# Performance work log

Hardware: AMD Instinct MI355X
Metric: run time of the kernel (lower is better)

## Reference

```python
import jax, jax.numpy as jnp
import numpy as np

T, B, D, N = 2048, 16, 1024, 128
EPS = 1e-6


def setup_inputs() -> dict:
    key = jax.random.key(0)
    ks = jax.random.split(key, 6)
    sc = 1.0 / np.sqrt(D)  # ~xavier scale for [N, D] projections
    x = jax.random.normal(ks[0], (T, B, D), jnp.float32)
    S = jnp.zeros((B, N, N), jnp.float32)
    W_k = jax.random.normal(ks[1], (N, D), jnp.float32) * sc
    W_v = jax.random.normal(ks[2], (N, D), jnp.float32) * sc
    W_q = jax.random.normal(ks[3], (N, D), jnp.float32) * sc
    W_beta = jax.random.normal(ks[4], (N, D), jnp.float32) * sc
    d_beta = jnp.full((N,), 0.1, jnp.float32)
    b_beta = jnp.zeros((N,), jnp.float32)
    return {"x": x, "S": S, "W_k": W_k, "W_v": W_v, "W_q": W_q,
            "W_beta": W_beta, "d_beta": d_beta, "b_beta": b_beta}


def reference(x, S, W_k, W_v, W_q, W_beta, d_beta, b_beta):
    # Batched input projections (dense GEMMs over all T*B tokens at once).
    k_all = jnp.einsum('tbd,nd->tbn', x, W_k)
    v_all = jnp.einsum('tbd,nd->tbn', x, W_v)
    q_all = jnp.einsum('tbd,nd->tbn', x, W_q)
    bx_all = jnp.einsum('tbd,nd->tbn', x, W_beta)

    def step(S, inp):
        k, v, q, bx = inp  # each [B, N]
        k_norm = k / (jnp.linalg.norm(k, axis=-1, keepdims=True) + EPS)
        retrieved = jnp.einsum('bij,bj->bi', S, k_norm)
        beta = jax.nn.sigmoid(bx + d_beta * retrieved + b_beta)
        # Delta rule: S += beta * outer(v - retrieved, k_norm)
        S = S + beta[..., None] * ((v - retrieved)[..., None] * k_norm[:, None, :])
        out = jnp.einsum('bij,bj->bi', S, q)
        out = out * jax.nn.silu(out)  # self-gated output
        return S, out

    S_final, outputs = jax.lax.scan(step, S, (k_all, v_all, q_all, bx_all))
    return outputs, S_final
```

## Files before the change

kernel.cpp:

```cpp
#include <hip/hip_runtime.h>
#include <hip/hip_bf16.h>


#define T_STEPS 2048
#define NB 16
#define ND 128
#define KD 1024
#define PSTRIDE 512

typedef __attribute__((ext_vector_type(4))) float f32x4;
typedef __attribute__((ext_vector_type(2))) float f32x2;
typedef __attribute__((ext_vector_type(8))) short short8v;

__device__ __forceinline__ unsigned short f2bf(float f) {
  union { float f; unsigned int u; } c; c.f = f;
  unsigned int u = c.u;
  unsigned int r = u + 0x7fffu + ((u >> 16) & 1u);
  return (unsigned short)(r >> 16);
}

__global__ __launch_bounds__(256) void proj_gemm(
    const float* __restrict__ X,
    const float* __restrict__ Wk, const float* __restrict__ Wv,
    const float* __restrict__ Wq, const float* __restrict__ Wb,
    float* __restrict__ C)
{
  __shared__ unsigned short As[128 * 64];
  __shared__ unsigned short Bs[128 * 64];
  const int tid = threadIdx.x;
  const int bm = blockIdx.x;
  const int bn = blockIdx.y;
  const float* W = (bn == 0) ? Wk : ((bn == 1) ? Wv : ((bn == 2) ? Wq : Wb));
  const int lane = tid & 63;
  const int wave = tid >> 6;
  const int wr = wave >> 1, wc = wave & 1;

  f32x4 acc[4][4];
#pragma unroll
  for (int i = 0; i < 4; i++)
#pragma unroll
    for (int j = 0; j < 4; j++) acc[i][j] = (f32x4){0.f, 0.f, 0.f, 0.f};

  for (int k0 = 0; k0 < KD; k0 += 64) {
    __syncthreads();
#pragma unroll
    for (int c = 0; c < 4; c++) {
      const int g = tid + c * 256;
      const int row = g >> 3;
      const int ch = g & 7;
      const int pos = ((ch ^ (row & 7)) * 8);
      {
        const float* ga = X + (size_t)(bm * 128 + row) * KD + k0 + ch * 8;
        float4 f0 = *(const float4*)(ga);
        float4 f1 = *(const float4*)(ga + 4);
        union { unsigned short u[8]; short8v v; } pk2;
        pk2.u[0] = f2bf(f0.x); pk2.u[1] = f2bf(f0.y);
        pk2.u[2] = f2bf(f0.z); pk2.u[3] = f2bf(f0.w);
        pk2.u[4] = f2bf(f1.x); pk2.u[5] = f2bf(f1.y);
        pk2.u[6] = f2bf(f1.z); pk2.u[7] = f2bf(f1.w);
        *reinterpret_cast<short8v*>(&As[row * 64 + pos]) = pk2.v;
      }
      {
        const float* gb = W + (size_t)row * KD + k0 + ch * 8;
        float4 f0 = *(const float4*)(gb);
        float4 f1 = *(const float4*)(gb + 4);
        union { unsigned short u[8]; short8v v; } pk2;
        pk2.u[0] = f2bf(f0.x); pk2.u[1] = f2bf(f0.y);
        pk2.u[2] = f2bf(f0.z); pk2.u[3] = f2bf(f0.w);
        pk2.u[4] = f2bf(f1.x); pk2.u[5] = f2bf(f1.y);
        pk2.u[6] = f2bf(f1.z); pk2.u[7] = f2bf(f1.w);
        *reinterpret_cast<short8v*>(&Bs[row * 64 + pos]) = pk2.v;
      }
    }
    __syncthreads();
#pragma unroll
    for (int kk = 0; kk < 2; kk++) {
      const int ch = kk * 4 + (lane >> 4);
      short8v a[4], b[4];
#pragma unroll
      for (int i = 0; i < 4; i++) {
        const int ar = wr * 64 + i * 16 + (lane & 15);
        a[i] = *reinterpret_cast<const short8v*>(&As[ar * 64 + ((ch ^ (ar & 7)) * 8)]);
        const int br = wc * 64 + i * 16 + (lane & 15);
        b[i] = *reinterpret_cast<const short8v*>(&Bs[br * 64 + ((ch ^ (br & 7)) * 8)]);
      }
#pragma unroll
      for (int i = 0; i < 4; i++)
#pragma unroll
        for (int j = 0; j < 4; j++)
          acc[i][j] = __builtin_amdgcn_mfma_f32_16x16x32_bf16(a[i], b[j], acc[i][j], 0, 0, 0);
    }
  }
#pragma unroll
  for (int i = 0; i < 4; i++)
#pragma unroll
    for (int j = 0; j < 4; j++)
#pragma unroll
      for (int r = 0; r < 4; r++) {
        const int row = bm * 128 + wr * 64 + i * 16 + (lane >> 4) * 4 + r;
        const int col = bn * 128 + wc * 64 + j * 16 + (lane & 15);
        C[(size_t)row * PSTRIDE + col] = acc[i][j][r];
      }
}

__global__ __launch_bounds__(256) void norm_k(float* __restrict__ proj) {
  const int lane = threadIdx.x & 63;
  const int wid = (blockIdx.x * 256 + threadIdx.x) >> 6;
  float* rowp = proj + (size_t)wid * PSTRIDE;
  float2 kv = *reinterpret_cast<float2*>(rowp + lane * 2);
  float ss = kv.x * kv.x + kv.y * kv.y;
  ss += __shfl_xor(ss, 1);
  ss += __shfl_xor(ss, 2);
  ss += __shfl_xor(ss, 4);
  ss += __shfl_xor(ss, 8);
  ss += __shfl_xor(ss, 16);
  ss += __shfl_xor(ss, 32);
  const float rn = 1.0f / (sqrtf(ss) + 1e-6f);
  kv.x *= rn; kv.y *= rn;
  *reinterpret_cast<float2*>(rowp + lane * 2) = kv;
}

__device__ __forceinline__ float sum16r(float v) {
  v += __int_as_float(__builtin_amdgcn_update_dpp(0, __float_as_int(v), 0x128, 0xF, 0xF, true));
  v += __int_as_float(__builtin_amdgcn_update_dpp(0, __float_as_int(v), 0x124, 0xF, 0xF, true));
  v += __int_as_float(__builtin_amdgcn_update_dpp(0, __float_as_int(v), 0x122, 0xF, 0xF, true));
  v += __int_as_float(__builtin_amdgcn_update_dpp(0, __float_as_int(v), 0x121, 0xF, 0xF, true));
  return v;
}

struct Buf { f32x4 kn0, kn1, q0, q1; float v, bx; };

__device__ __forceinline__ void load_buf_asm(const float* pk, const float* pv, Buf& b) {
  asm volatile("global_load_dwordx4 %0, %1, off"             : "=v"(b.kn0) : "v"(pk));
  asm volatile("global_load_dwordx4 %0, %1, off offset:16"   : "=v"(b.kn1) : "v"(pk));
  asm volatile("global_load_dwordx4 %0, %1, off offset:1024" : "=v"(b.q0)  : "v"(pk));
  asm volatile("global_load_dwordx4 %0, %1, off offset:1040" : "=v"(b.q1)  : "v"(pk));
  asm volatile("global_load_dword %0, %1, off offset:512"    : "=v"(b.v)   : "v"(pv));
  asm volatile("global_load_dword %0, %1, off offset:1536"   : "=v"(b.bx)  : "v"(pv));
}

__device__ __forceinline__ float core(const Buf& b, float db, float bb, f32x2 S2[4]) {
  const f32x2 k0 = {b.kn0.x, b.kn0.y}, k1 = {b.kn0.z, b.kn0.w};
  const f32x2 k2 = {b.kn1.x, b.kn1.y}, k3 = {b.kn1.z, b.kn1.w};
  f32x2 a0 = S2[0] * k0;
  f32x2 a1 = S2[1] * k1;
  a0 = __builtin_elementwise_fma(S2[2], k2, a0);
  a1 = __builtin_elementwise_fma(S2[3], k3, a1);
  const f32x2 ac = a0 + a1;
  const float r = sum16r(ac.x + ac.y);
  const float lg = fmaf(db, r, b.bx + bb);
  const float beta = __builtin_amdgcn_rcpf(1.0f + __expf(-lg));
  const float cr = beta * (b.v - r);
  const f32x2 cr2 = {cr, cr};
  S2[0] = __builtin_elementwise_fma(cr2, k0, S2[0]);
  S2[1] = __builtin_elementwise_fma(cr2, k1, S2[1]);
  S2[2] = __builtin_elementwise_fma(cr2, k2, S2[2]);
  S2[3] = __builtin_elementwise_fma(cr2, k3, S2[3]);
  const f32x2 q0 = {b.q0.x, b.q0.y}, q1 = {b.q0.z, b.q0.w};
  const f32x2 q2 = {b.q1.x, b.q1.y}, q3 = {b.q1.z, b.q1.w};
  f32x2 o0 = S2[0] * q0;
  f32x2 o1 = S2[1] * q1;
  o0 = __builtin_elementwise_fma(S2[2], q2, o0);
  o1 = __builtin_elementwise_fma(S2[3], q3, o1);
  const f32x2 ao = o0 + o1;
  return sum16r(ao.x + ao.y);
}

__device__ __forceinline__ float fin(float od) {
  return od * od * __builtin_amdgcn_rcpf(1.0f + __expf(-od));
}

__global__ __launch_bounds__(64) void scan_kernel(
    const float* __restrict__ proj, const float* __restrict__ S_in,
    const float* __restrict__ d_beta, const float* __restrict__ b_beta,
    float* __restrict__ out, float* __restrict__ S_out)
{
  const int lane = threadIdx.x & 63;
  const int batch = blockIdx.x & 15;
  const int grp = blockIdx.x >> 4;
  const int cc = lane & 15;
  const int rloc = lane >> 4;
  const int row = grp * 4 + rloc;
  const bool w0 = (cc == 0);

  f32x2 S2[4];
  {
    const f32x4* Sp4 = reinterpret_cast<const f32x4*>(
        S_in + ((size_t)batch * ND + row) * ND + cc * 8);
    const f32x4 s0 = Sp4[0], s1 = Sp4[1];
    S2[0] = (f32x2){s0.x, s0.y}; S2[1] = (f32x2){s0.z, s0.w};
    S2[2] = (f32x2){s1.x, s1.y}; S2[3] = (f32x2){s1.z, s1.w};
  }
  const float db = d_beta[row];
  const float bb = b_beta[row];

  const float* pb = proj + (size_t)batch * PSTRIDE;
  const float* pkb = pb + cc * 8;
  const float* pvb = pb + row;
  const size_t sstep = (size_t)NB * PSTRIDE;
  float* outp = out + (size_t)batch * ND + row;
  const size_t ostep = (size_t)NB * ND;

  Buf A, B, C, D;
  load_buf_asm(pkb + 0 * sstep, pvb + 0 * sstep, A);
  load_buf_asm(pkb + 1 * sstep, pvb + 1 * sstep, B);
  load_buf_asm(pkb + 2 * sstep, pvb + 2 * sstep, C);
  load_buf_asm(pkb + 3 * sstep, pvb + 3 * sstep, D);

  float od_prev;

#define WAIT18 do { asm volatile("s_waitcnt vmcnt(18)" ::: "memory"); \
                    __builtin_amdgcn_sched_barrier(0); } while (0)

#define SLOT(BUF, tnext)                                                  \
  do {                                                                    \
    const float gprev = fin(od_prev);                                     \
    if (w0) *outp = gprev;                                                \
    outp += ostep;                                                        \
    WAIT18;                                                               \
    od_prev = core(BUF, db, bb, S2);                                      \
    __builtin_amdgcn_sched_barrier(0);                                    \
    load_buf_asm(pkb + (size_t)(tnext) * sstep,                           \
                 pvb + (size_t)(tnext) * sstep, BUF);                     \
    __builtin_amdgcn_sched_barrier(0);                                    \
  } while (0)

  WAIT18;
  od_prev = core(A, db, bb, S2);
  __builtin_amdgcn_sched_barrier(0);
  load_buf_asm(pkb + 4 * sstep, pvb + 4 * sstep, A);
  __builtin_amdgcn_sched_barrier(0);
  SLOT(B, 5);
  SLOT(C, 6);
  SLOT(D, 7);

  for (int t = 4; t + 8 <= T_STEPS; t += 4) {
    SLOT(A, t + 4);
    SLOT(B, t + 5);
    SLOT(C, t + 6);
    SLOT(D, t + 7);
  }

  {
    const float g = fin(od_prev);
    if (w0) *outp = g;
    outp += ostep;
  }
  asm volatile("s_waitcnt vmcnt(0)" ::: "memory");
  __builtin_amdgcn_sched_barrier(0);
  od_prev = core(A, db, bb, S2);
  { const float g = fin(od_prev); if (w0) *outp = g; outp += ostep; }
  od_prev = core(B, db, bb, S2);
  { const float g = fin(od_prev); if (w0) *outp = g; outp += ostep; }
  od_prev = core(C, db, bb, S2);
  { const float g = fin(od_prev); if (w0) *outp = g; outp += ostep; }
  od_prev = core(D, db, bb, S2);
  { const float g = fin(od_prev); if (w0) *outp = g; }
#undef SLOT
#undef WAIT18

  {
    f32x4* So4 = reinterpret_cast<f32x4*>(
        S_out + ((size_t)batch * ND + row) * ND + cc * 8);
    f32x4 s0, s1;
    s0.x = S2[0].x; s0.y = S2[0].y; s0.z = S2[1].x; s0.w = S2[1].y;
    s1.x = S2[2].x; s1.y = S2[2].y; s1.z = S2[3].x; s1.w = S2[3].y;
    So4[0] = s0; So4[1] = s1;
  }
}

extern "C" void kernel_launch(void* const* d_in, const int* in_sizes, int n_in,
                              void* d_out, int out_size, void* d_ws, size_t ws_size,
                              hipStream_t stream) {
  const float* x  = (const float*)d_in[0];
  const float* S0 = (const float*)d_in[1];
  const float* Wk = (const float*)d_in[2];
  const float* Wv = (const float*)d_in[3];
  const float* Wq = (const float*)d_in[4];
  const float* Wb = (const float*)d_in[5];
  const float* db = (const float*)d_in[6];
  const float* bb = (const float*)d_in[7];
  float* out  = (float*)d_out;
  float* Sout = out + (size_t)T_STEPS * NB * ND;
  float* proj = (float*)d_ws;

  dim3 ggrid(256, 4);
  proj_gemm<<<ggrid, 256, 0, stream>>>(x, Wk, Wv, Wq, Wb, proj);
  norm_k<<<8192, 256, 0, stream>>>(proj);
  scan_kernel<<<512, 64, 0, stream>>>(proj, S0, db, bb, out, Sout);
}
```

Measured before the change: 406.9 us.

## Reassociate delta-rule recurrence to overlap next-step retrieval with current update

```diff
diff --git a/kernel.cpp b/kernel.cpp
--- a/kernel.cpp
+++ b/kernel.cpp
@@ -139,31 +139,26 @@
   asm volatile("global_load_dword %0, %1, off offset:1536"   : "=v"(b.bx)  : "v"(pv));
 }
 
-__device__ __forceinline__ float core(const Buf& b, float db, float bb, f32x2 S2[4]) {
-  const f32x2 k0 = {b.kn0.x, b.kn0.y}, k1 = {b.kn0.z, b.kn0.w};
-  const f32x2 k2 = {b.kn1.x, b.kn1.y}, k3 = {b.kn1.z, b.kn1.w};
-  f32x2 a0 = S2[0] * k0;
-  f32x2 a1 = S2[1] * k1;
-  a0 = __builtin_elementwise_fma(S2[2], k2, a0);
-  a1 = __builtin_elementwise_fma(S2[3], k3, a1);
-  const f32x2 ac = a0 + a1;
-  const float r = sum16r(ac.x + ac.y);
-  const float lg = fmaf(db, r, b.bx + bb);
-  const float beta = __builtin_amdgcn_rcpf(1.0f + __expf(-lg));
-  const float cr = beta * (b.v - r);
-  const f32x2 cr2 = {cr, cr};
-  S2[0] = __builtin_elementwise_fma(cr2, k0, S2[0]);
-  S2[1] = __builtin_elementwise_fma(cr2, k1, S2[1]);
-  S2[2] = __builtin_elementwise_fma(cr2, k2, S2[2]);
-  S2[3] = __builtin_elementwise_fma(cr2, k3, S2[3]);
-  const f32x2 q0 = {b.q0.x, b.q0.y}, q1 = {b.q0.z, b.q0.w};
-  const f32x2 q2 = {b.q1.x, b.q1.y}, q3 = {b.q1.z, b.q1.w};
-  f32x2 o0 = S2[0] * q0;
-  f32x2 o1 = S2[1] * q1;
-  o0 = __builtin_elementwise_fma(S2[2], q2, o0);
-  o1 = __builtin_elementwise_fma(S2[3], q3, o1);
-  const f32x2 ao = o0 + o1;
-  return sum16r(ao.x + ao.y);
+__device__ __forceinline__ float dot8(const f32x4& a0, const f32x4& a1,
+                                      const f32x4& b0, const f32x4& b1) {
+  const f32x2 ax = {a0.x, a0.y}, ay = {a0.z, a0.w}, az = {a1.x, a1.y}, aw = {a1.z, a1.w};
+  const f32x2 bx = {b0.x, b0.y}, by = {b0.z, b0.w}, bz = {b1.x, b1.y}, bw = {b1.z, b1.w};
+  f32x2 p = ax * bx;
+  f32x2 q = ay * by;
+  p = __builtin_elementwise_fma(az, bz, p);
+  q = __builtin_elementwise_fma(aw, bw, q);
+  const f32x2 s = p + q;
+  return s.x + s.y;
+}
+
+__device__ __forceinline__ float dot8S(const f32x2 S2[4], const f32x4& b0, const f32x4& b1) {
+  const f32x2 bx = {b0.x, b0.y}, by = {b0.z, b0.w}, bz = {b1.x, b1.y}, bw = {b1.z, b1.w};
+  f32x2 p = S2[0] * bx;
+  f32x2 q = S2[1] * by;
+  p = __builtin_elementwise_fma(S2[2], bz, p);
+  q = __builtin_elementwise_fma(S2[3], bw, q);
+  const f32x2 s = p + q;
+  return s.x + s.y;
 }
 
 __device__ __forceinline__ float fin(float od) {
@@ -201,64 +196,81 @@
   float* outp = out + (size_t)batch * ND + row;
   const size_t ostep = (size_t)NB * ND;
 
-  Buf A, B, C, D;
-  load_buf_asm(pkb + 0 * sstep, pvb + 0 * sstep, A);
-  load_buf_asm(pkb + 1 * sstep, pvb + 1 * sstep, B);
-  load_buf_asm(pkb + 2 * sstep, pvb + 2 * sstep, C);
-  load_buf_asm(pkb + 3 * sstep, pvb + 3 * sstep, D);
-
-  float od_prev;
-
-#define WAIT18 do { asm volatile("s_waitcnt vmcnt(18)" ::: "memory"); \
+  Buf B0, B1, B2, B3, B4, B5, B6, B7;
+  load_buf_asm(pkb + 0 * sstep, pvb + 0 * sstep, B0);
+  load_buf_asm(pkb + 1 * sstep, pvb + 1 * sstep, B1);
+  load_buf_asm(pkb + 2 * sstep, pvb + 2 * sstep, B2);
+  load_buf_asm(pkb + 3 * sstep, pvb + 3 * sstep, B3);
+  load_buf_asm(pkb + 4 * sstep, pvb + 4 * sstep, B4);
+  load_buf_asm(pkb + 5 * sstep, pvb + 5 * sstep, B5);
+  load_buf_asm(pkb + 6 * sstep, pvb + 6 * sstep, B6);
+  load_buf_asm(pkb + 7 * sstep, pvb + 7 * sstep, B7);
+
+#define WAIT36 do { asm volatile("s_waitcnt vmcnt(36)" ::: "memory"); \
                     __builtin_amdgcn_sched_barrier(0); } while (0)
 
-#define SLOT(BUF, tnext)                                                  \
+  WAIT36;
+  float pre0 = sum16r(dot8S(S2, B0.kn0, B0.kn1));
+  float kkp = 0.f, crp = 0.f;
+
+#define SLOT(CUR, NXT, tnext)                                             \
   do {                                                                    \
-    const float gprev = fin(od_prev);                                     \
-    if (w0) *outp = gprev;                                                \
+    WAIT36;                                                               \
+                       \
+    const float d_pre = dot8S(S2, NXT.kn0, NXT.kn1);                      \
+    const float d_sq  = dot8S(S2, CUR.q0, CUR.q1);                        \
+    const float d_kk  = dot8(CUR.kn0, CUR.kn1, NXT.kn0, NXT.kn1);         \
+    const float d_kq  = dot8(CUR.kn0, CUR.kn1, CUR.q0, CUR.q1);           \
+    const float pre1 = sum16r(d_pre);                                     \
+    const float Sq   = sum16r(d_sq);                                      \
+    const float kk   = sum16r(d_kk);                                      \
+    const float kq   = sum16r(d_kq);                                      \
+                                                        \
+    const float r  = fmaf(crp, kkp, pre0);                                \
+    const float lg = fmaf(db, r, CUR.bx + bb);                            \
+    const float beta = __builtin_amdgcn_rcpf(1.0f + __expf(-lg));         \
+    const float cr = beta * (CUR.v - r);                                  \
+                                         \
+    const float od = fmaf(cr, kq, Sq);                                    \
+    if (w0) *outp = fin(od);                                              \
     outp += ostep;                                                        \
-    WAIT18;                                                               \
-    od_prev = core(BUF, db, bb, S2);                                      \
-    __builtin_amdgcn_sched_barrier(0);                                    \
+                                                            \
+    {                                                                     \
+      const f32x2 cr2 = {cr, cr};                                         \
+      const f32x2 kx = {CUR.kn0.x, CUR.kn0.y}, ky = {CUR.kn0.z, CUR.kn0.w}; \
+      const f32x2 kz = {CUR.kn1.x, CUR.kn1.y}, kw = {CUR.kn1.z, CUR.kn1.w}; \
+      S2[0] = __builtin_elementwise_fma(cr2, kx, S2[0]);                  \
+      S2[1] = __builtin_elementwise_fma(cr2, ky, S2[1]);                  \
+      S2[2] = __builtin_elementwise_fma(cr2, kz, S2[2]);                  \
+      S2[3] = __builtin_elementwise_fma(cr2, kw, S2[3]);                  \
+    }                                                                     \
+    pre0 = pre1; kkp = kk; crp = cr;                                      \
     load_buf_asm(pkb + (size_t)(tnext) * sstep,                           \
-                 pvb + (size_t)(tnext) * sstep, BUF);                     \
-    __builtin_amdgcn_sched_barrier(0);                                    \
+                 pvb + (size_t)(tnext) * sstep, CUR);                     \
   } while (0)
 
-  WAIT18;
-  od_prev = core(A, db, bb, S2);
-  __builtin_amdgcn_sched_barrier(0);
-  load_buf_asm(pkb + 4 * sstep, pvb + 4 * sstep, A);
-  __builtin_amdgcn_sched_barrier(0);
-  SLOT(B, 5);
-  SLOT(C, 6);
-  SLOT(D, 7);
-
-  for (int t = 4; t + 8 <= T_STEPS; t += 4) {
-    SLOT(A, t + 4);
-    SLOT(B, t + 5);
-    SLOT(C, t + 6);
-    SLOT(D, t + 7);
+  for (int t = 0; t < T_STEPS; t += 8) {
+    const int t0 = (t +  8 < T_STEPS) ? t +  8 : T_STEPS - 1;
+    const int t1 = (t +  9 < T_STEPS) ? t +  9 : T_STEPS - 1;
+    const int t2 = (t + 10 < T_STEPS) ? t + 10 : T_STEPS - 1;
+    const int t3 = (t + 11 < T_STEPS) ? t + 11 : T_STEPS - 1;
+    const int t4 = (t + 12 < T_STEPS) ? t + 12 : T_STEPS - 1;
+    const int t5 = (t + 13 < T_STEPS) ? t + 13 : T_STEPS - 1;
+    const int t6 = (t + 14 < T_STEPS) ? t + 14 : T_STEPS - 1;
+    const int t7 = (t + 15 < T_STEPS) ? t + 15 : T_STEPS - 1;
+    SLOT(B0, B1, t0);
+    SLOT(B1, B2, t1);
+    SLOT(B2, B3, t2);
+    SLOT(B3, B4, t3);
+    SLOT(B4, B5, t4);
+    SLOT(B5, B6, t5);
+    SLOT(B6, B7, t6);
+    SLOT(B7, B0, t7);
   }
-
-  {
-    const float g = fin(od_prev);
-    if (w0) *outp = g;
-    outp += ostep;
-  }
+#undef SLOT
+#undef WAIT36
+
   asm volatile("s_waitcnt vmcnt(0)" ::: "memory");
-  __builtin_amdgcn_sched_barrier(0);
-  od_prev = core(A, db, bb, S2);
-  { const float g = fin(od_prev); if (w0) *outp = g; outp += ostep; }
-  od_prev = core(B, db, bb, S2);
-  { const float g = fin(od_prev); if (w0) *outp = g; outp += ostep; }
-  od_prev = core(C, db, bb, S2);
-  { const float g = fin(od_prev); if (w0) *outp = g; outp += ostep; }
-  od_prev = core(D, db, bb, S2);
-  { const float g = fin(od_prev); if (w0) *outp = g; }
-#undef SLOT
-#undef WAIT18
-
   {
     f32x4* So4 = reinterpret_cast<f32x4*>(
         S_out + ((size_t)batch * ND + row) * ND + cc * 8);
```

Result: slower. 426.0 us (+4.7%).

## Interleave two batches per scan wave and fold b_beta into norm kernel

Applied to the files above, without the earlier changes.

```diff
diff --git a/kernel.cpp b/kernel.cpp
--- a/kernel.cpp
+++ b/kernel.cpp
@@ -103,7 +103,8 @@
       }
 }
 
-__global__ __launch_bounds__(256) void norm_k(float* __restrict__ proj) {
+__global__ __launch_bounds__(256) void norm_k(float* __restrict__ proj,
+                                              const float* __restrict__ b_beta) {
   const int lane = threadIdx.x & 63;
   const int wid = (blockIdx.x * 256 + threadIdx.x) >> 6;
   float* rowp = proj + (size_t)wid * PSTRIDE;
@@ -118,6 +119,10 @@
   const float rn = 1.0f / (sqrtf(ss) + 1e-6f);
   kv.x *= rn; kv.y *= rn;
   *reinterpret_cast<float2*>(rowp + lane * 2) = kv;
+  float2 bx = *reinterpret_cast<float2*>(rowp + 384 + lane * 2);
+  const float2 bb = *reinterpret_cast<const float2*>(b_beta + lane * 2);
+  bx.x += bb.x; bx.y += bb.y;
+  *reinterpret_cast<float2*>(rowp + 384 + lane * 2) = bx;
 }
 
 __device__ __forceinline__ float sum16r(float v) {
@@ -130,16 +135,7 @@
 
 struct Buf { f32x4 kn0, kn1, q0, q1; float v, bx; };
 
-__device__ __forceinline__ void load_buf_asm(const float* pk, const float* pv, Buf& b) {
-  asm volatile("global_load_dwordx4 %0, %1, off"             : "=v"(b.kn0) : "v"(pk));
-  asm volatile("global_load_dwordx4 %0, %1, off offset:16"   : "=v"(b.kn1) : "v"(pk));
-  asm volatile("global_load_dwordx4 %0, %1, off offset:1024" : "=v"(b.q0)  : "v"(pk));
-  asm volatile("global_load_dwordx4 %0, %1, off offset:1040" : "=v"(b.q1)  : "v"(pk));
-  asm volatile("global_load_dword %0, %1, off offset:512"    : "=v"(b.v)   : "v"(pv));
-  asm volatile("global_load_dword %0, %1, off offset:1536"   : "=v"(b.bx)  : "v"(pv));
-}
-
-__device__ __forceinline__ float core(const Buf& b, float db, float bb, f32x2 S2[4]) {
+__device__ __forceinline__ float core(const Buf& b, float db, f32x2 S2[4]) {
   const f32x2 k0 = {b.kn0.x, b.kn0.y}, k1 = {b.kn0.z, b.kn0.w};
   const f32x2 k2 = {b.kn1.x, b.kn1.y}, k3 = {b.kn1.z, b.kn1.w};
   f32x2 a0 = S2[0] * k0;
@@ -148,7 +144,7 @@
   a1 = __builtin_elementwise_fma(S2[3], k3, a1);
   const f32x2 ac = a0 + a1;
   const float r = sum16r(ac.x + ac.y);
-  const float lg = fmaf(db, r, b.bx + bb);
+  const float lg = fmaf(db, r, b.bx);
   const float beta = __builtin_amdgcn_rcpf(1.0f + __expf(-lg));
   const float cr = beta * (b.v - r);
   const f32x2 cr2 = {cr, cr};
@@ -170,102 +166,139 @@
   return od * od * __builtin_amdgcn_rcpf(1.0f + __expf(-od));
 }
 
-__global__ __launch_bounds__(64) void scan_kernel(
+#define ADVB 131072u
+
+__global__ __launch_bounds__(64)
+__attribute__((amdgpu_waves_per_eu(1, 1)))
+void scan_kernel(
     const float* __restrict__ proj, const float* __restrict__ S_in,
-    const float* __restrict__ d_beta, const float* __restrict__ b_beta,
+    const float* __restrict__ d_beta,
     float* __restrict__ out, float* __restrict__ S_out)
 {
   const int lane = threadIdx.x & 63;
-  const int batch = blockIdx.x & 15;
-  const int grp = blockIdx.x >> 4;
+  const int batchA = blockIdx.x & 7;
+  const int batchB = batchA + 8;
+  const int grp = blockIdx.x >> 3;
   const int cc = lane & 15;
   const int rloc = lane >> 4;
   const int row = grp * 4 + rloc;
   const bool w0 = (cc == 0);
 
-  f32x2 S2[4];
+  f32x2 S2A[4], S2B[4];
   {
-    const f32x4* Sp4 = reinterpret_cast<const f32x4*>(
-        S_in + ((size_t)batch * ND + row) * ND + cc * 8);
-    const f32x4 s0 = Sp4[0], s1 = Sp4[1];
-    S2[0] = (f32x2){s0.x, s0.y}; S2[1] = (f32x2){s0.z, s0.w};
-    S2[2] = (f32x2){s1.x, s1.y}; S2[3] = (f32x2){s1.z, s1.w};
+    const f32x4* SpA = reinterpret_cast<const f32x4*>(
+        S_in + ((size_t)batchA * ND + row) * ND + cc * 8);
+    const f32x4 a0 = SpA[0], a1 = SpA[1];
+    S2A[0] = (f32x2){a0.x, a0.y}; S2A[1] = (f32x2){a0.z, a0.w};
+    S2A[2] = (f32x2){a1.x, a1.y}; S2A[3] = (f32x2){a1.z, a1.w};
+    const f32x4* SpB = reinterpret_cast<const f32x4*>(
+        S_in + ((size_t)batchB * ND + row) * ND + cc * 8);
+    const f32x4 b0 = SpB[0], b1 = SpB[1];
+    S2B[0] = (f32x2){b0.x, b0.y}; S2B[1] = (f32x2){b0.z, b0.w};
+    S2B[2] = (f32x2){b1.x, b1.y}; S2B[3] = (f32x2){b1.z, b1.w};
   }
   const float db = d_beta[row];
-  const float bb = b_beta[row];
-
-  const float* pb = proj + (size_t)batch * PSTRIDE;
-  const float* pkb = pb + cc * 8;
-  const float* pvb = pb + row;
-  const size_t sstep = (size_t)NB * PSTRIDE;
-  float* outp = out + (size_t)batch * ND + row;
+
+  float* outpA = out + (size_t)batchA * ND + row;
+  float* outpB = out + (size_t)batchB * ND + row;
   const size_t ostep = (size_t)NB * ND;
 
-  Buf A, B, C, D;
-  load_buf_asm(pkb + 0 * sstep, pvb + 0 * sstep, A);
-  load_buf_asm(pkb + 1 * sstep, pvb + 1 * sstep, B);
-  load_buf_asm(pkb + 2 * sstep, pvb + 2 * sstep, C);
-  load_buf_asm(pkb + 3 * sstep, pvb + 3 * sstep, D);
-
-  float od_prev;
-
-#define WAIT18 do { asm volatile("s_waitcnt vmcnt(18)" ::: "memory"); \
+  const unsigned kbA = (unsigned)(batchA * PSTRIDE + cc * 8) * 4u;
+  const unsigned vbA = (unsigned)(batchA * PSTRIDE + 128 + row) * 4u;
+  const unsigned kbB = (unsigned)(batchB * PSTRIDE + cc * 8) * 4u;
+  const unsigned vbB = (unsigned)(batchB * PSTRIDE + 128 + row) * 4u;
+  const unsigned sst = (unsigned)(NB * PSTRIDE) * 4u;
+  unsigned kA0 = kbA + 0 * sst, kA1 = kbA + 1 * sst, kA2 = kbA + 2 * sst, kA3 = kbA + 3 * sst;
+  unsigned vA0 = vbA + 0 * sst, vA1 = vbA + 1 * sst, vA2 = vbA + 2 * sst, vA3 = vbA + 3 * sst;
+  unsigned kB0 = kbB + 0 * sst, kB1 = kbB + 1 * sst, kB2 = kbB + 2 * sst, kB3 = kbB + 3 * sst;
+  unsigned vB0 = vbB + 0 * sst, vB1 = vbB + 1 * sst, vB2 = vbB + 2 * sst, vB3 = vbB + 3 * sst;
+
+  Buf BA0, BA1, BA2, BA3, BB0, BB1, BB2, BB3;
+
+#define LOADB(B, KO, VO)                                                       \
+  do {                                                                         \
+    asm volatile("global_load_dwordx4 %0, %1, %2"             : "=v"((B).kn0) : "v"(KO), "s"(proj)); \
+    asm volatile("global_load_dwordx4 %0, %1, %2 offset:16"   : "=v"((B).kn1) : "v"(KO), "s"(proj)); \
+    asm volatile("global_load_dwordx4 %0, %1, %2 offset:1024" : "=v"((B).q0)  : "v"(KO), "s"(proj)); \
+    asm volatile("global_load_dwordx4 %0, %1, %2 offset:1040" : "=v"((B).q1)  : "v"(KO), "s"(proj)); \
+    asm volatile("global_load_dword %0, %1, %2"               : "=v"((B).v)   : "v"(VO), "s"(proj)); \
+    asm volatile("global_load_dword %0, %1, %2 offset:1024"   : "=v"((B).bx)  : "v"(VO), "s"(proj)); \
+    KO += ADVB; VO += ADVB;                                                    \
+  } while (0)
+
+  LOADB(BA0, kA0, vA0); LOADB(BB0, kB0, vB0);
+  LOADB(BA1, kA1, vA1); LOADB(BB1, kB1, vB1);
+  LOADB(BA2, kA2, vA2); LOADB(BB2, kB2, vB2);
+  LOADB(BA3, kA3, vA3); LOADB(BB3, kB3, vB3);
+
+#define WAIT36 do { asm volatile("s_waitcnt vmcnt(36)" ::: "memory"); \
                     __builtin_amdgcn_sched_barrier(0); } while (0)
 
-#define SLOT(BUF, tnext)                                                  \
+  float odA, odB;
+
+#define SLOT(i)                                                           \
   do {                                                                    \
-    const float gprev = fin(od_prev);                                     \
-    if (w0) *outp = gprev;                                                \
-    outp += ostep;                                                        \
-    WAIT18;                                                               \
-    od_prev = core(BUF, db, bb, S2);                                      \
-    __builtin_amdgcn_sched_barrier(0);                                    \
-    load_buf_asm(pkb + (size_t)(tnext) * sstep,                           \
-                 pvb + (size_t)(tnext) * sstep, BUF);                     \
+    { const float g = fin(odA); if (w0) *outpA = g; outpA += ostep; }     \
+    { const float g = fin(odB); if (w0) *outpB = g; outpB += ostep; }     \
+    WAIT36;                                                               \
+    odA = core(BA##i, db, S2A);                                           \
+    odB = core(BB##i, db, S2B);                                           \
+    LOADB(BA##i, kA##i, vA##i);                                           \
+    LOADB(BB##i, kB##i, vB##i);                                           \
     __builtin_amdgcn_sched_barrier(0);                                    \
   } while (0)
 
-  WAIT18;
-  od_prev = core(A, db, bb, S2);
+  WAIT36;
+  odA = core(BA0, db, S2A);
+  odB = core(BB0, db, S2B);
+  LOADB(BA0, kA0, vA0);
+  LOADB(BB0, kB0, vB0);
   __builtin_amdgcn_sched_barrier(0);
-  load_buf_asm(pkb + 4 * sstep, pvb + 4 * sstep, A);
-  __builtin_amdgcn_sched_barrier(0);
-  SLOT(B, 5);
-  SLOT(C, 6);
-  SLOT(D, 7);
-
-  for (int t = 4; t + 8 <= T_STEPS; t += 4) {
-    SLOT(A, t + 4);
-    SLOT(B, t + 5);
-    SLOT(C, t + 6);
-    SLOT(D, t + 7);
+  SLOT(1);
+  SLOT(2);
+  SLOT(3);
+
+  for (int t = 4; t < T_STEPS - 4; t += 4) {
+    SLOT(0);
+    SLOT(1);
+    SLOT(2);
+    SLOT(3);
   }
 
-  {
-    const float g = fin(od_prev);
-    if (w0) *outp = g;
-    outp += ostep;
-  }
+  { const float g = fin(odA); if (w0) *outpA = g; outpA += ostep; }
+  { const float g = fin(odB); if (w0) *outpB = g; outpB += ostep; }
   asm volatile("s_waitcnt vmcnt(0)" ::: "memory");
   __builtin_amdgcn_sched_barrier(0);
-  od_prev = core(A, db, bb, S2);
-  { const float g = fin(od_prev); if (w0) *outp = g; outp += ostep; }
-  od_prev = core(B, db, bb, S2);
-  { const float g = fin(od_prev); if (w0) *outp = g; outp += ostep; }
-  od_prev = core(C, db, bb, S2);
-  { const float g = fin(od_prev); if (w0) *outp = g; outp += ostep; }
-  od_prev = core(D, db, bb, S2);
-  { const float g = fin(od_prev); if (w0) *outp = g; }
+
+#define TAIL(i)                                                           \
+  do {                                                                    \
+    odA = core(BA##i, db, S2A);                                           \
+    { const float g = fin(odA); if (w0) *outpA = g; outpA += ostep; }     \
+    odB = core(BB##i, db, S2B);                                           \
+    { const float g = fin(odB); if (w0) *outpB = g; outpB += ostep; }     \
+  } while (0)
+  TAIL(0);
+  TAIL(1);
+  TAIL(2);
+  TAIL(3);
+#undef TAIL
 #undef SLOT
-#undef WAIT18
+#undef WAIT36
+#undef LOADB
 
   {
-    f32x4* So4 = reinterpret_cast<f32x4*>(
-        S_out + ((size_t)batch * ND + row) * ND + cc * 8);
+    f32x4* SoA = reinterpret_cast<f32x4*>(
+        S_out + ((size_t)batchA * ND + row) * ND + cc * 8);
     f32x4 s0, s1;
-    s0.x = S2[0].x; s0.y = S2[0].y; s0.z = S2[1].x; s0.w = S2[1].y;
-    s1.x = S2[2].x; s1.y = S2[2].y; s1.z = S2[3].x; s1.w = S2[3].y;
-    So4[0] = s0; So4[1] = s1;
+    s0.x = S2A[0].x; s0.y = S2A[0].y; s0.z = S2A[1].x; s0.w = S2A[1].y;
+    s1.x = S2A[2].x; s1.y = S2A[2].y; s1.z = S2A[3].x; s1.w = S2A[3].y;
+    SoA[0] = s0; SoA[1] = s1;
+    f32x4* SoB = reinterpret_cast<f32x4*>(
+        S_out + ((size_t)batchB * ND + row) * ND + cc * 8);
+    f32x4 t0, t1;
+    t0.x = S2B[0].x; t0.y = S2B[0].y; t0.z = S2B[1].x; t0.w = S2B[1].y;
+    t1.x = S2B[2].x; t1.y = S2B[2].y; t1.z = S2B[3].x; t1.w = S2B[3].y;
+    SoB[0] = t0; SoB[1] = t1;
   }
 }
 
@@ -286,6 +319,6 @@
 
   dim3 ggrid(256, 4);
   proj_gemm<<<ggrid, 256, 0, stream>>>(x, Wk, Wv, Wq, Wb, proj);
-  norm_k<<<8192, 256, 0, stream>>>(proj);
-  scan_kernel<<<512, 64, 0, stream>>>(proj, S0, db, bb, out, Sout);
-}
+  norm_k<<<8192, 256, 0, stream>>>(proj, bb);
+  scan_kernel<<<256, 64, 0, stream>>>(proj, S0, db, out, Sout);
+}
```

Result: slower. 657.5 us (+61.6%).
